# Performance work log

Hardware: AMD Instinct MI355X
Metric: run time of the kernel (lower is better)

The kernel has to match this reference:

```python
import jax, jax.numpy as jnp
import numpy as np

NUM_CLASSES = 41
EPS = 1e-12


def nearest_resize(lab, h, w):
    # torch F.interpolate(mode='nearest'): src_idx = floor(dst_idx * in / out)
    Hl, Wl = lab.shape[1], lab.shape[2]
    ih = (jnp.arange(h) * Hl) // h
    iw = (jnp.arange(w) * Wl) // w
    return lab[:, ih][:, :, iw]


def segment_mean(feats, lab_small, base):
    # feats [b,c,h,w], lab_small [b,h,w] int, base [b,L,c] (values for absent labels)
    b, c, h, w = feats.shape
    L = NUM_CLASSES
    lab = lab_small.reshape(b, h * w)
    ids = (jnp.arange(b, dtype=lab.dtype)[:, None] * L + lab).reshape(-1)  # [b*h*w]
    x = feats.reshape(b, c, h * w).transpose(0, 2, 1).reshape(-1, c)       # [b*h*w, c]
    sums = jax.ops.segment_sum(x, ids, num_segments=b * L).reshape(b, L, c)
    cnts = jax.ops.segment_sum(jnp.ones((b * h * w,), feats.dtype), ids,
                               num_segments=b * L).reshape(b, L, 1)
    mean = sums / jnp.maximum(cnts, 1.0)
    return jnp.where(cnts > 0, mean, base)


def ra_gate(feats, lab_small, base, w1, w2):
    # RA.forward: segment-mean queue -> L2 normalize over class dim -> sum -> 1x1 convs -> sigmoid
    att = segment_mean(feats, lab_small, base)                      # [b,L,c]
    nrm = jnp.sqrt(jnp.sum(att * att, axis=1, keepdims=True))       # over classes (dim=1)
    att = att / jnp.maximum(nrm, EPS)
    s = jnp.sum(att, axis=1)                                        # [b,c]
    h1 = jax.nn.relu(jnp.einsum('bc,oc->bo', s, w1))                # conv1 1x1, no bias
    g = jax.nn.sigmoid(jnp.einsum('bo,co->bc', h1, w2))             # conv2 1x1, no bias
    return g[:, :, None, None]                                      # [b,c,1,1]


def conv3x3(x, w):
    return jax.lax.conv_general_dilated(
        x, w, window_strides=(1, 1), padding=((1, 1), (1, 1)),
        dimension_numbers=('NCHW', 'OIHW', 'NCHW'))


def setup_inputs() -> dict:
    key = jax.random.key(0)
    ks = jax.random.split(key, 10)
    B, C, H, W = 8, 128, 128, 128
    return {
        'r': jax.random.normal(ks[0], (B, C, H, W), jnp.float32),
        'd': jax.random.normal(ks[1], (B, C, H, W), jnp.float32),
        'label': jax.random.randint(ks[2], (B, 4 * H, 4 * W), 0, NUM_CLASSES, jnp.int32),
        'conv_w': jax.random.normal(ks[3], (C, 2 * C, 3, 3), jnp.float32) * 0.05,
        'f_w1': jax.random.normal(ks[4], (C // 16, C), jnp.float32) * 0.05,
        'f_w2': jax.random.normal(ks[5], (C, C // 16), jnp.float32) * 0.05,
        'd_w1': jax.random.normal(ks[6], (C // 16, C), jnp.float32) * 0.05,
        'd_w2': jax.random.normal(ks[7], (C, C // 16), jnp.float32) * 0.05,
        'seg_base_f': jax.random.normal(ks[8], (B, NUM_CLASSES, C), jnp.float32),
        'seg_base_d': jax.random.normal(ks[9], (B, NUM_CLASSES, C), jnp.float32),
    }


def reference(r, d, label, conv_w, f_w1, f_w2, d_w1, d_w2, seg_base_f, seg_base_d):
    b, c, h, w = r.shape
    add = r + d
    mul = r * jax.nn.sigmoid(d)
    fuse = conv3x3(jnp.concatenate([add, mul], axis=1), conv_w)
    lab_small = nearest_resize(label, h, w)
    d_ra = d * ra_gate(d, lab_small, seg_base_d, d_w1, d_w2)
    fuse_ra = fuse * ra_gate(fuse, lab_small, seg_base_f, f_w1, f_w2)
    return fuse_ra + d_ra
```

## Files before the change

### kernel.cpp

```cpp
#include <hip/hip_runtime.h>
#include <math.h>

typedef unsigned short u16;
typedef unsigned char u8;
typedef unsigned int u32;
typedef unsigned long long u64;
typedef __bf16 bf16x8 __attribute__((ext_vector_type(8)));
typedef float f32x4 __attribute__((ext_vector_type(4)));

#define NL 41
#define HW 16384

#define NHWC_OFF   0
#define WA_OFF     67108864
#define LAB8_OFF   67698688
#define GHIST_OFF  67829760
#define SUMS_OFF   67833856
#define GATES_OFF  68169728
#define PF_OFF     68177920
#define PF_END     78925824ull

#define PSZ 5248

__device__ __forceinline__ u16 f2bf(float f) {
    u32 u = __builtin_bit_cast(u32, f);
    u = (u + 0x7FFFu + ((u >> 16) & 1u)) >> 16;
    return (u16)u;
}

__device__ __forceinline__ void glds16(const void* g, void* l) {
    __builtin_amdgcn_global_load_lds(
        (const __attribute__((address_space(1))) void*)g,
        (__attribute__((address_space(3))) void*)l, 16, 0, 0);
}

__global__ __launch_bounds__(64)
void k_wpack(const float* __restrict__ w, u16* __restrict__ wa,
             int* __restrict__ ghist)
{
    const int bid = (int)blockIdx.x;
    const int l = (int)threadIdx.x;
    if (bid == 0) {
        for (int i = l; i < 8 * NL; i += 64) ghist[i] = 0;
    }
    const int kt = bid >> 3, ct = bid & 7;
    const int chunk = kt / 9, tap = kt - chunk * 9;
    const int co = ct * 16 + (l & 15);
    const int cin0 = chunk * 32 + (l >> 4) * 8;
    u16 tmp[8];
#pragma unroll
    for (int j = 0; j < 8; ++j)
        tmp[j] = f2bf(w[((size_t)co * 256 + cin0 + j) * 9 + tap]);
    *(f32x4*)&wa[((size_t)bid * 64 + l) * 8] = *(f32x4*)tmp;
}

__global__ __launch_bounds__(256, 2)
void k_prep(const float* __restrict__ r, const float* __restrict__ d,
            const int* __restrict__ label, u16* __restrict__ nhwc,
            u8* __restrict__ lab8, int* __restrict__ ghist,
            float* __restrict__ pd)
{
    __shared__ u16 s[64 * 256];
    __shared__ float binsd[NL * 256];
    __shared__ int hist[NL];
    __shared__ u8 s_lab[256];
    const int bid = (int)blockIdx.x;
    const int b = bid >> 6;
    const int px0 = (bid & 63) * 256;
    const int tid = (int)threadIdx.x;
    const int c = tid & 127;
    const int half = tid >> 7;

    if (tid < NL) hist[tid] = 0;
    for (int i = tid; i < NL * 64; i += 256) ((f32x4*)binsd)[i] = f32x4{0,0,0,0};
    __syncthreads();

    {
        int px = px0 + tid;
        int yy = px >> 7, xx = px & 127;
        int lab = label[(size_t)b * 512 * 512 + (yy * 4) * 512 + xx * 4];
        lab8[b * HW + px] = (u8)lab;
        s_lab[tid] = (u8)lab;
        atomicAdd(&hist[lab], 1);
    }
    __syncthreads();

    for (int t = 0; t < 4; ++t) {
        const int pxb = px0 + t * 64 + half * 32;
        const float* rp = r + ((size_t)(b * 128 + c)) * HW + pxb;
        const float* dp = d + ((size_t)(b * 128 + c)) * HW + pxb;
        const u8* lp = &s_lab[t * 64 + half * 32];
        uint4 lw0 = *(const uint4*)lp;
        uint4 lw1 = *(const uint4*)(lp + 16);
        u32 lwords[8] = {lw0.x, lw0.y, lw0.z, lw0.w, lw1.x, lw1.y, lw1.z, lw1.w};
#pragma unroll
        for (int j = 0; j < 8; ++j) {
            float4 rv = *(const float4*)(rp + j * 4);
            float4 dv = *(const float4*)(dp + j * 4);
            float ra[4] = {rv.x, rv.y, rv.z, rv.w};
            float da[4] = {dv.x, dv.y, dv.z, dv.w};
#pragma unroll
            for (int i = 0; i < 4; ++i) {
                int pxl = half * 32 + j * 4 + i;
                s[pxl * 256 + c] = f2bf(ra[i] + da[i]);
                s[pxl * 256 + 128 + c] = f2bf(ra[i] / (1.f + __expf(-da[i])));
                int lab = (int)((lwords[j] >> (i * 8)) & 0xffu);
                binsd[lab * 256 + tid] += da[i];
            }
        }
        __syncthreads();
        const f32x4* sf = (const f32x4*)s;
        f32x4* dst = (f32x4*)nhwc + ((size_t)b * HW + px0 + t * 64) * 32;
#pragma unroll
        for (int k = 0; k < 8; ++k) {
            int fi = k * 256 + tid;
            dst[fi] = sf[fi];
        }
        __syncthreads();
    }
    float* pout = pd + (size_t)bid * PSZ;
    for (int i = tid; i < NL * 128; i += 256) {
        int lab = i >> 7, cc = i & 127;
        pout[i] = binsd[lab * 256 + cc] + binsd[lab * 256 + 128 + cc];
    }
    if (tid < NL && hist[tid] > 0) atomicAdd(&ghist[b * NL + tid], hist[tid]);
}

template<int EP>
__global__ __launch_bounds__(256, 2)
void k_conv(const u16* __restrict__ nhwc, const u16* __restrict__ wa,
            const u8* __restrict__ lab8, float* __restrict__ out,
            float* __restrict__ pf)
{
    __shared__ u16 s_in[2 * 2080 * 8];
    __shared__ u8 s_lab[256];
    const int tid = (int)threadIdx.x;
    const int bid = (int)blockIdx.x;
    const int b = bid & 7;
    const int y0 = (bid >> 3) * 2;
    const int l = tid & 63;
    const int wv = tid >> 6;
    const int wr = wv & 1;
    const int wc = wv >> 1;
    const int l15 = l & 15;
    const int l16 = l >> 4;

    {
        f32x4 zz = {0.f, 0.f, 0.f, 0.f};
        for (int i = tid; i < 4160; i += 256) ((f32x4*)s_in)[i] = zz;
    }
    if (EP) s_lab[tid] = lab8[b * HW + y0 * 128 + tid];

    int goff[9];
#pragma unroll
    for (int it = 0; it < 9; ++it) {
        int s = it * 256 + tid;
        int row = s / 520;
        int rem = s - row * 520;
        int xslot = rem >> 2;
        int ci8 = rem & 3;
        int gy = y0 - 1 + row;
        int gx = xslot - 1;
        bool valid = (s < 2080) && ((unsigned)gy < 128u) && ((unsigned)gx < 128u);
        goff[it] = valid ? (((gy << 7) | gx) * 256 + ci8 * 8) * 2 : -1;
    }

    f32x4 acc[4][8];
#pragma unroll
    for (int i = 0; i < 4; ++i)
#pragma unroll
        for (int j = 0; j < 8; ++j) {
            f32x4 zz = {0.f, 0.f, 0.f, 0.f};
            acc[i][j] = zz;
        }

    const char* src_b = (const char*)(nhwc + (size_t)b * HW * 256);
    const int lane_base = (tid & 192) * 16;
    const f32x4* wa4 = (const f32x4*)wa;

    __syncthreads();
#pragma unroll
    for (int it = 0; it < 9; ++it)
        if (goff[it] >= 0)
            glds16(src_b + goff[it], (char*)s_in + it * 4096 + lane_base);

#pragma unroll 1
    for (int chunk = 0; chunk < 8; ++chunk) {
        __syncthreads();

        f32x4 a0[4], a1[4];
        {
            int kt8 = chunk * 72;
#pragma unroll
            for (int i = 0; i < 4; ++i) a0[i] = wa4[(kt8 + wc * 4 + i) * 64 + l];
#pragma unroll
            for (int i = 0; i < 4; ++i) a1[i] = wa4[(kt8 + 8 + wc * 4 + i) * 64 + l];
        }
        if (chunk < 7) {
            char* dstb = (char*)s_in + ((chunk + 1) & 1) * 33280 + lane_base;
#pragma unroll
            for (int it = 0; it < 9; ++it)
                if (goff[it] >= 0)
                    glds16(src_b + goff[it] + (chunk + 1) * 64, dstb + it * 4096);
        }

        const char* bufp = (const char*)s_in + (chunk & 1) * 33280;
#pragma unroll
        for (int tap = 0; tap < 9; ++tap) {
            f32x4 aC[4];
#pragma unroll
            for (int i = 0; i < 4; ++i) aC[i] = a0[i];
#pragma unroll
            for (int i = 0; i < 4; ++i) a0[i] = a1[i];
            if (tap + 2 < 9) {
                int kt8 = chunk * 72 + (tap + 2) * 8;
#pragma unroll
                for (int i = 0; i < 4; ++i)
                    a1[i] = wa4[(kt8 + wc * 4 + i) * 64 + l];
            }
            const int rowi = wr + tap / 3;
            const int dxo = tap % 3;
            f32x4 bf[8];
#pragma unroll
            for (int p = 0; p < 8; ++p) {
                int e = (rowi * 130 + p * 16 + l15 + dxo) * 64 + l16 * 16;
                bf[p] = *(const f32x4*)(bufp + e);
            }
#pragma unroll
            for (int ct = 0; ct < 4; ++ct) {
                bf16x8 av = __builtin_bit_cast(bf16x8, aC[ct]);
#pragma unroll
                for (int p = 0; p < 8; ++p)
                    acc[ct][p] = __builtin_amdgcn_mfma_f32_16x16x32_bf16(
                        av, __builtin_bit_cast(bf16x8, bf[p]), acc[ct][p], 0, 0, 0);
            }
        }
    }

    const int y = y0 + wr;
    float* outb = out + (size_t)b * 128 * HW + (size_t)y * 128;
#pragma unroll
    for (int ct = 0; ct < 4; ++ct)
#pragma unroll
        for (int p = 0; p < 8; ++p) {
            int x = p * 16 + l15;
#pragma unroll
            for (int rr = 0; rr < 4; ++rr) {
                int co = wc * 64 + ct * 16 + l16 * 4 + rr;
                outb[(size_t)co * HW + x] = acc[ct][p][rr];
            }
        }

    if (EP) {
        __syncthreads();
        float* binsf = (float*)s_in;
        for (int i = tid; i < 2 * NL * 129; i += 256) binsf[i] = 0.f;
        __syncthreads();
#pragma unroll
        for (int ct = 0; ct < 4; ++ct)
#pragma unroll
            for (int p = 0; p < 8; ++p) {
                int lab = (int)s_lab[wr * 128 + p * 16 + l15];
                float* bp = &binsf[(wr * NL + lab) * 129 + wc * 64 + ct * 16 + l16 * 4];
#pragma unroll
                for (int rr = 0; rr < 4; ++rr)
                    atomicAdd(bp + rr, acc[ct][p][rr]);
            }
        __syncthreads();
        float* pout = pf + (size_t)bid * PSZ;
        for (int i = tid; i < NL * 128; i += 256) {
            int lab = i >> 7, cc = i & 127;
            pout[i] = binsf[lab * 129 + cc] + binsf[(NL + lab) * 129 + cc];
        }
    }
}

__global__ __launch_bounds__(128)
void k_red(const float* __restrict__ p, float* __restrict__ sout,
           int bstride, int kstride)
{
    const int bid = (int)blockIdx.x;
    const int b = bid / 41, lab = bid - b * 41;
    const int c = (int)threadIdx.x;
    const float* q = p + (size_t)b * bstride + lab * 128 + c;
    float s = 0.f;
#pragma unroll 8
    for (int k = 0; k < 64; ++k) s += q[(size_t)k * kstride];
    sout[(size_t)bid * 128 + c] = s;
}

__global__ __launch_bounds__(256, 3)
void k_seg_f(const float* __restrict__ fuse, const u8* __restrict__ lab8,
             float* __restrict__ sums)
{
    __shared__ float bins[NL][256];
    const int bid = (int)blockIdx.x;
    const int c = bid & 127;
    const int b = bid >> 7;
    const int tid = (int)threadIdx.x;

    for (int i = tid; i < NL * 256; i += 256) ((float*)bins)[i] = 0.f;
    __syncthreads();

    const float* src = fuse + ((size_t)(b * 128 + c)) * HW;
    const u8* lp = lab8 + b * HW;

#pragma unroll 4
    for (int k = 0; k < 16; ++k) {
        int i = k * 256 + tid;
        float4 v = ((const float4*)src)[i];
        uchar4 lv = ((const uchar4*)lp)[i];
        bins[lv.x][tid] += v.x;
        bins[lv.y][tid] += v.y;
        bins[lv.z][tid] += v.z;
        bins[lv.w][tid] += v.w;
    }
    __syncthreads();

    for (int stride = 128; stride >= 1; stride >>= 1) {
        for (int idx = tid; idx < NL * stride; idx += 256) {
            int l = idx / stride;
            int cc = idx - l * stride;
            bins[l][cc] += bins[l][cc + stride];
        }
        __syncthreads();
    }
    if (tid < NL)
        sums[(size_t)(b * NL + tid) * 128 + c] = bins[tid][0];
}

__global__ __launch_bounds__(128)
void k_gates(const float* __restrict__ sums, const int* __restrict__ ghist,
             const float* __restrict__ base_f, const float* __restrict__ base_d,
             const float* __restrict__ f_w1, const float* __restrict__ f_w2,
             const float* __restrict__ d_w1, const float* __restrict__ d_w2,
             float* __restrict__ gates)
{
    __shared__ float sv[128];
    __shared__ float h1[8];
    const int b = (int)blockIdx.x >> 1;
    const int feat = (int)blockIdx.x & 1;
    const int c = (int)threadIdx.x;

    const float* base = feat ? base_d : base_f;
    const float* sf = sums + (size_t)feat * 8 * NL * 128;
    float suma = 0.f, sumsq = 0.f;
    for (int lc = 0; lc < NL; ++lc) {
        float s = sf[(size_t)(b * NL + lc) * 128 + c];
        int cnt = ghist[b * NL + lc];
        float att = (cnt > 0) ? (s / (float)cnt) : base[(b * NL + lc) * 128 + c];
        suma += att;
        sumsq += att * att;
    }
    sv[c] = suma / fmaxf(sqrtf(sumsq), 1e-12f);
    __syncthreads();

    const float* w1 = feat ? d_w1 : f_w1;
    const float* w2 = feat ? d_w2 : f_w2;
    if (c < 8) {
        float h = 0.f;
        for (int k = 0; k < 128; ++k) h += w1[c * 128 + k] * sv[k];
        h1[c] = fmaxf(h, 0.f);
    }
    __syncthreads();

    float gv = 0.f;
#pragma unroll
    for (int o = 0; o < 8; ++o) gv += w2[c * 8 + o] * h1[o];
    gates[feat * 1024 + b * 128 + c] = 1.f / (1.f + expf(-gv));
}

__global__ __launch_bounds__(256)
void k_final(const float* __restrict__ d, const float* __restrict__ gates,
             float* out)
{
    size_t t4 = (size_t)blockIdx.x * 256 + threadIdx.x;
    size_t basei = t4 * 4;
    int bc = (int)(basei >> 14);
    float gf = gates[bc];
    float gd = gates[1024 + bc];
    float4 f = *(const float4*)(out + basei);
    float4 dv = *(const float4*)(d + basei);
    float4 o;
    o.x = f.x * gf + dv.x * gd;
    o.y = f.y * gf + dv.y * gd;
    o.z = f.z * gf + dv.z * gd;
    o.w = f.w * gf + dv.w * gd;
    *(float4*)(out + basei) = o;
}

extern "C" void kernel_launch(void* const* d_in, const int* in_sizes, int n_in,
                              void* d_out, int out_size, void* d_ws, size_t ws_size,
                              hipStream_t stream)
{
    (void)in_sizes; (void)n_in; (void)out_size;
    const float* r      = (const float*)d_in[0];
    const float* d      = (const float*)d_in[1];
    const int*   label  = (const int*)d_in[2];
    const float* conv_w = (const float*)d_in[3];
    const float* f_w1   = (const float*)d_in[4];
    const float* f_w2   = (const float*)d_in[5];
    const float* d_w1   = (const float*)d_in[6];
    const float* d_w2   = (const float*)d_in[7];
    const float* base_f = (const float*)d_in[8];
    const float* base_d = (const float*)d_in[9];
    float* out = (float*)d_out;

    char* ws = (char*)d_ws;
    u16* nhwc    = (u16*)(ws + NHWC_OFF);
    u16* wa      = (u16*)(ws + WA_OFF);
    u8*  lab8    = (u8*)(ws + LAB8_OFF);
    int* ghist   = (int*)(ws + GHIST_OFF);
    float* sums  = (float*)(ws + SUMS_OFF);
    float* sums_f = sums;
    float* sums_d = sums + 8 * NL * 128;
    float* gates = (float*)(ws + GATES_OFF);
    float* pf    = (float*)(ws + PF_OFF);
    float* pd    = (float*)d_out;

    const bool big = ws_size >= PF_END;

    hipLaunchKernelGGL(k_wpack, dim3(576), dim3(64), 0, stream, conv_w, wa, ghist);
    hipLaunchKernelGGL(k_prep, dim3(512), dim3(256), 0, stream, r, d, label,
                       nhwc, lab8, ghist, pd);
    hipLaunchKernelGGL(k_red, dim3(328), dim3(128), 0, stream, pd, sums_d,
                       64 * PSZ, PSZ);
    if (big) {
        hipLaunchKernelGGL(k_conv<1>, dim3(512), dim3(256), 0, stream, nhwc, wa,
                           lab8, out, pf);
        hipLaunchKernelGGL(k_red, dim3(328), dim3(128), 0, stream, pf, sums_f,
                           PSZ, 8 * PSZ);
    } else {
        hipLaunchKernelGGL(k_conv<0>, dim3(512), dim3(256), 0, stream, nhwc, wa,
                           lab8, out, (float*)nullptr);
        hipLaunchKernelGGL(k_seg_f, dim3(1024), dim3(256), 0, stream, out,
                           lab8, sums_f);
    }
    hipLaunchKernelGGL(k_gates, dim3(16), dim3(128), 0, stream, sums, ghist,
                       base_f, base_d, f_w1, f_w2, d_w1, d_w2, gates);
    hipLaunchKernelGGL(k_final, dim3(16384), dim3(256), 0, stream, d, gates, out);
}
```

Before: 428.8 us.

## Fold weight packing into prep, drop conv-epilogue binning, recompute histograms in gates

Weight packing moves into the first 144 blocks of k_prep, and the label histogram is no longer built with global atomics. Instead k_gates recomputes each batch's label counts from lab8 in shared memory. The conv epilogue's per-block segment binning is removed. The feature segment sums now always come from a separate k_seg2 pass over the conv output, which also does the d-reduction in extra blocks. k_final processes eight float4s per thread. This cuts kernel launches and atomics, but it re-reads the full conv output for segmentation, whereas before that work was fused into the conv epilogue.

```diff
diff --git a/kernel.cpp b/kernel.cpp
--- a/kernel.cpp
+++ b/kernel.cpp
@@ -14,11 +14,10 @@
 #define NHWC_OFF   0
 #define WA_OFF     67108864
 #define LAB8_OFF   67698688
-#define GHIST_OFF  67829760
-#define SUMS_OFF   67833856
-#define GATES_OFF  68169728
-#define PF_OFF     68177920
-#define PF_END     78925824ull
+#define SUMS_OFF   67829760
+#define GATES_OFF  68165632
+#define PD_OFF     68173824
+#define PD_END     78921728ull
 
 #define PSZ 5248
 
@@ -34,35 +33,14 @@
         (__attribute__((address_space(3))) void*)l, 16, 0, 0);
 }
 
-__global__ __launch_bounds__(64)
-void k_wpack(const float* __restrict__ w, u16* __restrict__ wa,
-             int* __restrict__ ghist)
-{
-    const int bid = (int)blockIdx.x;
-    const int l = (int)threadIdx.x;
-    if (bid == 0) {
-        for (int i = l; i < 8 * NL; i += 64) ghist[i] = 0;
-    }
-    const int kt = bid >> 3, ct = bid & 7;
-    const int chunk = kt / 9, tap = kt - chunk * 9;
-    const int co = ct * 16 + (l & 15);
-    const int cin0 = chunk * 32 + (l >> 4) * 8;
-    u16 tmp[8];
-#pragma unroll
-    for (int j = 0; j < 8; ++j)
-        tmp[j] = f2bf(w[((size_t)co * 256 + cin0 + j) * 9 + tap]);
-    *(f32x4*)&wa[((size_t)bid * 64 + l) * 8] = *(f32x4*)tmp;
-}
-
 __global__ __launch_bounds__(256, 2)
 void k_prep(const float* __restrict__ r, const float* __restrict__ d,
-            const int* __restrict__ label, u16* __restrict__ nhwc,
-            u8* __restrict__ lab8, int* __restrict__ ghist,
-            float* __restrict__ pd)
+            const int* __restrict__ label, const float* __restrict__ w,
+            u16* __restrict__ nhwc, u16* __restrict__ wa,
+            u8* __restrict__ lab8, float* __restrict__ pd)
 {
     __shared__ u16 s[64 * 256];
     __shared__ float binsd[NL * 256];
-    __shared__ int hist[NL];
     __shared__ u8 s_lab[256];
     const int bid = (int)blockIdx.x;
     const int b = bid >> 6;
@@ -71,9 +49,21 @@
     const int c = tid & 127;
     const int half = tid >> 7;
 
-    if (tid < NL) hist[tid] = 0;
+    if (bid < 144) {
+        const int wi = bid * 4 + (tid >> 6);
+        const int l = tid & 63;
+        const int kt = wi >> 3, ct = wi & 7;
+        const int chunk = kt / 9, tap = kt - chunk * 9;
+        const int co = ct * 16 + (l & 15);
+        const int cin0 = chunk * 32 + (l >> 4) * 8;
+        u16 tmp[8];
+#pragma unroll
+        for (int j = 0; j < 8; ++j)
+            tmp[j] = f2bf(w[((size_t)co * 256 + cin0 + j) * 9 + tap]);
+        *(f32x4*)&wa[((size_t)wi * 64 + l) * 8] = *(f32x4*)tmp;
+    }
+
     for (int i = tid; i < NL * 64; i += 256) ((f32x4*)binsd)[i] = f32x4{0,0,0,0};
-    __syncthreads();
 
     {
         int px = px0 + tid;
@@ -81,7 +71,6 @@
         int lab = label[(size_t)b * 512 * 512 + (yy * 4) * 512 + xx * 4];
         lab8[b * HW + px] = (u8)lab;
         s_lab[tid] = (u8)lab;
-        atomicAdd(&hist[lab], 1);
     }
     __syncthreads();
 
@@ -123,17 +112,13 @@
         int lab = i >> 7, cc = i & 127;
         pout[i] = binsd[lab * 256 + cc] + binsd[lab * 256 + 128 + cc];
     }
-    if (tid < NL && hist[tid] > 0) atomicAdd(&ghist[b * NL + tid], hist[tid]);
-}
-
-template<int EP>
+}
+
 __global__ __launch_bounds__(256, 2)
 void k_conv(const u16* __restrict__ nhwc, const u16* __restrict__ wa,
-            const u8* __restrict__ lab8, float* __restrict__ out,
-            float* __restrict__ pf)
+            float* __restrict__ out)
 {
     __shared__ u16 s_in[2 * 2080 * 8];
-    __shared__ u8 s_lab[256];
     const int tid = (int)threadIdx.x;
     const int bid = (int)blockIdx.x;
     const int b = bid & 7;
@@ -149,7 +134,6 @@
         f32x4 zz = {0.f, 0.f, 0.f, 0.f};
         for (int i = tid; i < 4160; i += 256) ((f32x4*)s_in)[i] = zz;
     }
-    if (EP) s_lab[tid] = lab8[b * HW + y0 * 128 + tid];
 
     int goff[9];
 #pragma unroll
@@ -250,54 +234,32 @@
                 outb[(size_t)co * HW + x] = acc[ct][p][rr];
             }
         }
-
-    if (EP) {
-        __syncthreads();
-        float* binsf = (float*)s_in;
-        for (int i = tid; i < 2 * NL * 129; i += 256) binsf[i] = 0.f;
-        __syncthreads();
-#pragma unroll
-        for (int ct = 0; ct < 4; ++ct)
-#pragma unroll
-            for (int p = 0; p < 8; ++p) {
-                int lab = (int)s_lab[wr * 128 + p * 16 + l15];
-                float* bp = &binsf[(wr * NL + lab) * 129 + wc * 64 + ct * 16 + l16 * 4];
-#pragma unroll
-                for (int rr = 0; rr < 4; ++rr)
-                    atomicAdd(bp + rr, acc[ct][p][rr]);
-            }
-        __syncthreads();
-        float* pout = pf + (size_t)bid * PSZ;
-        for (int i = tid; i < NL * 128; i += 256) {
-            int lab = i >> 7, cc = i & 127;
-            pout[i] = binsf[lab * 129 + cc] + binsf[(NL + lab) * 129 + cc];
-        }
-    }
-}
-
-__global__ __launch_bounds__(128)
-void k_red(const float* __restrict__ p, float* __restrict__ sout,
-           int bstride, int kstride)
-{
-    const int bid = (int)blockIdx.x;
-    const int b = bid / 41, lab = bid - b * 41;
-    const int c = (int)threadIdx.x;
-    const float* q = p + (size_t)b * bstride + lab * 128 + c;
-    float s = 0.f;
-#pragma unroll 8
-    for (int k = 0; k < 64; ++k) s += q[(size_t)k * kstride];
-    sout[(size_t)bid * 128 + c] = s;
 }
 
 __global__ __launch_bounds__(256, 3)
-void k_seg_f(const float* __restrict__ fuse, const u8* __restrict__ lab8,
-             float* __restrict__ sums)
+void k_seg2(const float* __restrict__ fuse, const float* __restrict__ pd,
+            const u8* __restrict__ lab8, float* __restrict__ sums_f,
+            float* __restrict__ sums_d)
 {
     __shared__ float bins[NL][256];
     const int bid = (int)blockIdx.x;
+    const int tid = (int)threadIdx.x;
+
+    if (bid >= 1024) {
+        const int idx = bid - 1024;
+        if (tid < 128) {
+            const int b = idx / 41, lab = idx - b * 41;
+            const float* q = pd + (size_t)b * 64 * PSZ + lab * 128 + tid;
+            float sv = 0.f;
+#pragma unroll 8
+            for (int k = 0; k < 64; ++k) sv += q[(size_t)k * PSZ];
+            sums_d[(size_t)idx * 128 + tid] = sv;
+        }
+        return;
+    }
+
     const int c = bid & 127;
     const int b = bid >> 7;
-    const int tid = (int)threadIdx.x;
 
     for (int i = tid; i < NL * 256; i += 256) ((float*)bins)[i] = 0.f;
     __syncthreads();
@@ -326,11 +288,11 @@
         __syncthreads();
     }
     if (tid < NL)
-        sums[(size_t)(b * NL + tid) * 128 + c] = bins[tid][0];
+        sums_f[(size_t)(b * NL + tid) * 128 + c] = bins[tid][0];
 }
 
 __global__ __launch_bounds__(128)
-void k_gates(const float* __restrict__ sums, const int* __restrict__ ghist,
+void k_gates(const float* __restrict__ sums, const u8* __restrict__ lab8,
              const float* __restrict__ base_f, const float* __restrict__ base_d,
              const float* __restrict__ f_w1, const float* __restrict__ f_w2,
              const float* __restrict__ d_w1, const float* __restrict__ d_w2,
@@ -338,16 +300,31 @@
 {
     __shared__ float sv[128];
     __shared__ float h1[8];
+    __shared__ int hist[NL];
     const int b = (int)blockIdx.x >> 1;
     const int feat = (int)blockIdx.x & 1;
     const int c = (int)threadIdx.x;
+
+    if (c < NL) hist[c] = 0;
+    __syncthreads();
+    {
+        const uchar4* lp = (const uchar4*)(lab8 + (size_t)b * HW);
+        for (int k = 0; k < 32; ++k) {
+            uchar4 lv = lp[c + k * 128];
+            atomicAdd(&hist[lv.x], 1);
+            atomicAdd(&hist[lv.y], 1);
+            atomicAdd(&hist[lv.z], 1);
+            atomicAdd(&hist[lv.w], 1);
+        }
+    }
+    __syncthreads();
 
     const float* base = feat ? base_d : base_f;
     const float* sf = sums + (size_t)feat * 8 * NL * 128;
     float suma = 0.f, sumsq = 0.f;
     for (int lc = 0; lc < NL; ++lc) {
         float s = sf[(size_t)(b * NL + lc) * 128 + c];
-        int cnt = ghist[b * NL + lc];
+        int cnt = hist[lc];
         float att = (cnt > 0) ? (s / (float)cnt) : base[(b * NL + lc) * 128 + c];
         suma += att;
         sumsq += att * att;
@@ -374,19 +351,36 @@
 void k_final(const float* __restrict__ d, const float* __restrict__ gates,
              float* out)
 {
-    size_t t4 = (size_t)blockIdx.x * 256 + threadIdx.x;
-    size_t basei = t4 * 4;
-    int bc = (int)(basei >> 14);
-    float gf = gates[bc];
-    float gd = gates[1024 + bc];
-    float4 f = *(const float4*)(out + basei);
-    float4 dv = *(const float4*)(d + basei);
-    float4 o;
-    o.x = f.x * gf + dv.x * gd;
-    o.y = f.y * gf + dv.y * gd;
-    o.z = f.z * gf + dv.z * gd;
-    o.w = f.w * gf + dv.w * gd;
-    *(float4*)(out + basei) = o;
+    const size_t base = (size_t)blockIdx.x * 256 + threadIdx.x;
+#pragma unroll
+    for (int it = 0; it < 8; ++it) {
+        size_t t4 = base + (size_t)it * (2048 * 256);
+        size_t basei = t4 * 4;
+        int bc = (int)(basei >> 14);
+        float gf = gates[bc];
+        float gd = gates[1024 + bc];
+        float4 f = *(const float4*)(out + basei);
+        float4 dv = *(const float4*)(d + basei);
+        float4 o;
+        o.x = f.x * gf + dv.x * gd;
+        o.y = f.y * gf + dv.y * gd;
+        o.z = f.z * gf + dv.z * gd;
+        o.w = f.w * gf + dv.w * gd;
+        *(float4*)(out + basei) = o;
+    }
+}
+
+__global__ __launch_bounds__(128)
+void k_red(const float* __restrict__ p, float* __restrict__ sout)
+{
+    const int bid = (int)blockIdx.x;
+    const int b = bid / 41, lab = bid - b * 41;
+    const int c = (int)threadIdx.x;
+    const float* q = p + (size_t)b * 64 * PSZ + lab * 128 + c;
+    float s = 0.f;
+#pragma unroll 8
+    for (int k = 0; k < 64; ++k) s += q[(size_t)k * PSZ];
+    sout[(size_t)bid * 128 + c] = s;
 }
 
 extern "C" void kernel_launch(void* const* d_in, const int* in_sizes, int n_in,
@@ -407,36 +401,25 @@
     float* out = (float*)d_out;
 
     char* ws = (char*)d_ws;
-    u16* nhwc    = (u16*)(ws + NHWC_OFF);
-    u16* wa      = (u16*)(ws + WA_OFF);
-    u8*  lab8    = (u8*)(ws + LAB8_OFF);
-    int* ghist   = (int*)(ws + GHIST_OFF);
-    float* sums  = (float*)(ws + SUMS_OFF);
+    u16* nhwc     = (u16*)(ws + NHWC_OFF);
+    u16* wa       = (u16*)(ws + WA_OFF);
+    u8*  lab8     = (u8*)(ws + LAB8_OFF);
+    float* sums   = (float*)(ws + SUMS_OFF);
     float* sums_f = sums;
     float* sums_d = sums + 8 * NL * 128;
-    float* gates = (float*)(ws + GATES_OFF);
-    float* pf    = (float*)(ws + PF_OFF);
-    float* pd    = (float*)d_out;
-
-    const bool big = ws_size >= PF_END;
-
-    hipLaunchKernelGGL(k_wpack, dim3(576), dim3(64), 0, stream, conv_w, wa, ghist);
+    float* gates  = (float*)(ws + GATES_OFF);
+
+    const bool big = ws_size >= PD_END;
+    float* pd = big ? (float*)(ws + PD_OFF) : (float*)d_out;
+
     hipLaunchKernelGGL(k_prep, dim3(512), dim3(256), 0, stream, r, d, label,
-                       nhwc, lab8, ghist, pd);
-    hipLaunchKernelGGL(k_red, dim3(328), dim3(128), 0, stream, pd, sums_d,
-                       64 * PSZ, PSZ);
-    if (big) {
-        hipLaunchKernelGGL(k_conv<1>, dim3(512), dim3(256), 0, stream, nhwc, wa,
-                           lab8, out, pf);
-        hipLaunchKernelGGL(k_red, dim3(328), dim3(128), 0, stream, pf, sums_f,
-                           PSZ, 8 * PSZ);
-    } else {
-        hipLaunchKernelGGL(k_conv<0>, dim3(512), dim3(256), 0, stream, nhwc, wa,
-                           lab8, out, (float*)nullptr);
-        hipLaunchKernelGGL(k_seg_f, dim3(1024), dim3(256), 0, stream, out,
-                           lab8, sums_f);
-    }
-    hipLaunchKernelGGL(k_gates, dim3(16), dim3(128), 0, stream, sums, ghist,
+                       conv_w, nhwc, wa, lab8, pd);
+    if (!big)
+        hipLaunchKernelGGL(k_red, dim3(328), dim3(128), 0, stream, pd, sums_d);
+    hipLaunchKernelGGL(k_conv, dim3(512), dim3(256), 0, stream, nhwc, wa, out);
+    hipLaunchKernelGGL(k_seg2, dim3(big ? 1352 : 1024), dim3(256), 0, stream,
+                       out, pd, lab8, sums_f, sums_d);
+    hipLaunchKernelGGL(k_gates, dim3(16), dim3(128), 0, stream, sums, lab8,
                        base_f, base_d, f_w1, f_w2, d_w1, d_w2, gates);
-    hipLaunchKernelGGL(k_final, dim3(16384), dim3(256), 0, stream, d, gates, out);
-}
+    hipLaunchKernelGGL(k_final, dim3(2048), dim3(256), 0, stream, d, gates, out);
+}
```

Result: faster. 368.5 us (-14.1%).
